# Kernel tuning notes

Hardware: AMD Instinct MI355X
Metric: run time of the kernel (lower is better)

Reference implementation:

```python
import jax, jax.numpy as jnp
import numpy as np

KG_E = 50000
KG_R = 500
E_DIM = 300
NE = 400000      # entity-entity adjacency nnz
NEER = 400000    # entity-entity-relation triples
ALPHA1 = 0.1
ALPHA2 = 0.3
LRELU_ALPHA = 0.2


def setup_inputs() -> dict:
    key = jax.random.key(0)
    ks = jax.random.split(key, 13)
    primal_e_0 = jax.random.normal(ks[0], (KG_E, E_DIM), jnp.float32)
    # sparse-ish relation->entity incidence matrices (dense storage as in torch code)
    r_head = (jax.random.uniform(ks[1], (KG_R, KG_E)) < 0.01).astype(jnp.float32)
    r_tail = (jax.random.uniform(ks[2], (KG_R, KG_E)) < 0.01).astype(jnp.float32)
    e_adj_index = jax.random.randint(ks[3], (2, NE), 0, KG_E)
    e_adj_data = jax.random.uniform(ks[4], (NE,), jnp.float32)
    eer_adj_index = jax.random.randint(ks[5], (2, NEER), 0, KG_E)
    eer_adj_data = jax.random.randint(ks[6], (NEER,), 0, KG_R)
    s = 0.05
    be_L = jax.random.normal(ks[7], (KG_E, 1), jnp.float32) * s
    be_R = jax.random.normal(ks[8], (KG_E, 1), jnp.float32) * s
    atten_r = jax.random.normal(ks[9], (2 * E_DIM, 1), jnp.float32) * s
    gcnW1 = jax.random.normal(ks[10], (E_DIM, E_DIM), jnp.float32) * s
    highwayWr = jax.random.normal(ks[11], (E_DIM, E_DIM), jnp.float32) * s
    highwaybr = jax.random.normal(ks[12], (E_DIM, 1), jnp.float32) * s
    return {"primal_e_0": primal_e_0, "r_head": r_head, "r_tail": r_tail,
            "e_adj_data": e_adj_data, "be_L": be_L, "be_R": be_R,
            "atten_r": atten_r, "gcnW1": gcnW1, "highwayWr": highwayWr,
            "highwaybr": highwaybr, "e_adj_index": e_adj_index,
            "eer_adj_index": eer_adj_index, "eer_adj_data": eer_adj_data}


def _spmm(idx, data, x):
    # sparse [KG_E, KG_E] (COO rows=idx[0], cols=idx[1], vals=data) @ dense x
    rows, cols = idx[0], idx[1]
    return jax.ops.segment_sum(data[:, None] * x[cols], rows, num_segments=KG_E)


def _inv_or_zero(x):
    return jnp.where(x == 0, 0.0, 1.0 / x)


def _add_r_layer(e, be_L, be_R, r_head, r_tail, rh_inv, rt_inv):
    L_r = (r_head @ (e * be_L)) * rh_inv   # [KG_R, E_DIM]
    R_r = (r_tail @ (e * be_R)) * rt_inv
    return jax.nn.relu(jnp.concatenate([L_r, R_r], axis=-1))  # [KG_R, 2*E_DIM]


def _add_e_att_layer(e, r_layer, eer_idx, eer_rel, atten_r):
    rows, cols = eer_idx[0], eer_idx[1]
    e_ij = jnp.concatenate([e[rows], e[cols]], axis=1)           # [NEER, 2*E_DIM]
    eer_embed = e_ij * r_layer[eer_rel]                           # [NEER, 2*E_DIM]
    score = (eer_embed @ atten_r)[:, 0]                           # [NEER]
    ee_atten = jnp.exp(-jax.nn.leaky_relu(score, LRELU_ALPHA))
    e_rowsum = jax.ops.segment_sum(ee_atten, rows, num_segments=KG_E)[:, None]
    e_rowsum = _inv_or_zero(e_rowsum)
    e_out = jax.ops.segment_sum(ee_atten[:, None] * e[cols], rows, num_segments=KG_E)
    return jax.nn.relu(e_out * e_rowsum)


def _add_diag_layer(e, gcnW1, e_adj_index, e_adj_data):
    # dropout p=0 (eval) -> identity
    return jax.nn.relu(_spmm(e_adj_index, e_adj_data, e @ gcnW1))


def _highway(e1, e2, Wr, br):
    gate = jax.nn.sigmoid(e1 @ Wr + br[:, 0])
    return gate * e2 + (1.0 - gate) * e1


def reference(primal_e_0, r_head, r_tail, e_adj_data, be_L, be_R, atten_r,
              gcnW1, highwayWr, highwaybr, e_adj_index, eer_adj_index,
              eer_adj_data):
    rh_inv = _inv_or_zero(jnp.sum(r_head, axis=-1, keepdims=True))
    rt_inv = _inv_or_zero(jnp.sum(r_tail, axis=-1, keepdims=True))
    name_embed = primal_e_0
    r1 = _add_r_layer(name_embed, be_L, be_R, r_head, r_tail, rh_inv, rt_inv)
    e1 = _add_e_att_layer(name_embed, r1, eer_adj_index, eer_adj_data, atten_r)
    e1 = name_embed + ALPHA1 * e1
    r2 = _add_r_layer(e1, be_L, be_R, r_head, r_tail, rh_inv, rt_inv)
    e2 = _add_e_att_layer(e1, r2, eer_adj_index, eer_adj_data, atten_r)
    e2 = name_embed + ALPHA2 * e2
    g1 = _add_diag_layer(e2, gcnW1, e_adj_index, e_adj_data)
    g2 = _highway(e2, g1, highwayWr, highwaybr)
    g3 = _add_diag_layer(g2, gcnW1, e_adj_index, e_adj_data)
    return _highway(g2, g3, highwayWr, highwaybr)
```

## Files before the change

kernel.cpp:

```cpp
#include <hip/hip_runtime.h>
#include <hip/hip_fp16.h>
#include <math.h>

#define KG_E  50000
#define KG_R  500
#define E_DIM 300
#define NPAIR 150
#define NP2   75
#define CAP   1024
#define LRELU 0.2f

#define NK    10
#define NT    40
#define XS_LD 328

#define NB_SCAN 49

typedef __attribute__((ext_vector_type(8))) _Float16 f16x8;
typedef __attribute__((ext_vector_type(4))) float f32x4;

__device__ __forceinline__ __half2 u2h2(unsigned u) {
  union { unsigned u; __half2 h; } v; v.u = u; return v.h;
}
__device__ __forceinline__ unsigned h22u(__half2 h) {
  union { unsigned u; __half2 h; } v; v.h = h; return v.u;
}
__device__ __forceinline__ float hlo(unsigned u) { return __low2float(u2h2(u)); }
__device__ __forceinline__ float hhi(unsigned u) { return __high2float(u2h2(u)); }
__device__ __forceinline__ unsigned packh(float lo, float hi) {
  return h22u(__floats2half2_rn(lo, hi));
}

__global__ __launch_bounds__(256) void k_toh(
    const float* __restrict__ src, __half* __restrict__ dst, int n4)
{
  int i = blockIdx.x * 256 + threadIdx.x;
  if (i >= n4) return;
  float4 f = ((const float4*)src)[i];
  uint2 o;
  o.x = packh(f.x, f.y);
  o.y = packh(f.z, f.w);
  ((uint2*)dst)[i] = o;
}

#define NCH 5
#define SCAP 1024
#define NF4 2500
__global__ __launch_bounds__(256) void k_compact2(
    const float* __restrict__ r_head, const float* __restrict__ r_tail,
    const float* __restrict__ be_L, const float* __restrict__ be_R,
    int* __restrict__ lidx, float* __restrict__ lsval,
    int* __restrict__ fill, float* __restrict__ rsum)
{
  __shared__ int   ls_e[SCAP];
  __shared__ float ls_v[SCAP];
  __shared__ int   ls_cnt;
  __shared__ float ls_sum;
  __shared__ int   ls_base;
  int m = blockIdx.z;
  int r = blockIdx.y;
  const float* rowp = (m ? r_tail : r_head) + (size_t)r * KG_E;
  const float* be   = m ? be_R : be_L;
  int slot = m * KG_R + r;
  int lane = threadIdx.x & 63;
  if (threadIdx.x == 0) { ls_cnt = 0; ls_sum = 0.f; }
  __syncthreads();

  const int CH = KG_E / NCH;
  int c0 = blockIdx.x * CH;
  const float4* rp4 = (const float4*)(rowp + c0);

  float vals[48];
  #pragma unroll
  for (int t = 0; t < 12; ++t) {
    int fi = t * 256 + threadIdx.x;
    float4 f = (fi < NF4) ? rp4[fi] : make_float4(0.f, 0.f, 0.f, 0.f);
    vals[t*4+0] = f.x; vals[t*4+1] = f.y; vals[t*4+2] = f.z; vals[t*4+3] = f.w;
  }
  float lsum = 0.f;
  int cnt = 0;
  #pragma unroll
  for (int q = 0; q < 48; ++q) {
    lsum += vals[q];
    cnt += (vals[q] != 0.f) ? 1 : 0;
  }
  int pre = cnt;
  #pragma unroll
  for (int off = 1; off < 64; off <<= 1) {
    int u = __shfl_up(pre, off, 64);
    if (lane >= off) pre += u;
  }
  int wave_base = 0;
  if (lane == 63 && pre > 0) wave_base = atomicAdd(&ls_cnt, pre);
  wave_base = __shfl(wave_base, 63, 64);
  if (cnt > 0) {
    int o = wave_base + pre - cnt;
    #pragma unroll
    for (int t = 0; t < 12; ++t) {
      int fi = t * 256 + threadIdx.x;
      #pragma unroll
      for (int q = 0; q < 4; ++q) {
        float v = vals[t*4+q];
        if (v != 0.f) {
          if (o < SCAP) {
            int e = c0 + fi * 4 + q;
            ls_e[o] = e;
            ls_v[o] = v * be[e];
          }
          ++o;
        }
      }
    }
  }
  #pragma unroll
  for (int off = 32; off > 0; off >>= 1) lsum += __shfl_xor(lsum, off, 64);
  if (lane == 0 && lsum != 0.f) atomicAdd(&ls_sum, lsum);
  __syncthreads();

  int total = ls_cnt < SCAP ? ls_cnt : SCAP;
  if (threadIdx.x == 0) {
    ls_base = atomicAdd(&fill[slot], total);
    if (ls_sum != 0.f) atomicAdd(&rsum[slot], ls_sum);
  }
  __syncthreads();
  int gbase = ls_base;
  int*   li = lidx  + (size_t)slot * CAP;
  float* lv = lsval + (size_t)slot * CAP;
  for (int i = threadIdx.x; i < total; i += 256) {
    int pos = gbase + i;
    if (pos < CAP) { li[pos] = ls_e[i]; lv[pos] = ls_v[i]; }
  }
}

__global__ __launch_bounds__(256) void k_rmeta(
    const int* __restrict__ fill, const float* __restrict__ rsum,
    int* __restrict__ cnt, float* __restrict__ inv)
{
  int i = blockIdx.x * 256 + threadIdx.x;
  if (i < 2 * KG_R) {
    int c = fill[i];
    cnt[i] = c > CAP ? CAP : c;
    float s = rsum[i];
    inv[i] = (s == 0.f) ? 0.f : 1.f / s;
  }
}

__global__ __launch_bounds__(192) void k_rlayer(
    const __half* __restrict__ Eb, const int* __restrict__ lidx,
    const float* __restrict__ lsval, const int* __restrict__ cnt,
    const float* __restrict__ inv, const float* __restrict__ atten,
    unsigned* __restrict__ wpk)
{
  int b = blockIdx.x;
  int m = b / KG_R, r = b % KG_R;
  int p = threadIdx.x;
  if (p >= NPAIR) return;
  int slot = m * KG_R + r;
  int n = cnt[slot];
  const int*   li = lidx  + (size_t)slot * CAP;
  const float* lv = lsval + (size_t)slot * CAP;
  float alo = 0.f, ahi = 0.f;
  #pragma unroll 4
  for (int i = 0; i < n; ++i) {
    int e = li[i];
    float s = lv[i];
    unsigned u = ((const unsigned*)(Eb + (size_t)e * E_DIM))[p];
    alo += s * hlo(u);
    ahi += s * hhi(u);
  }
  float iv = inv[slot];
  float vlo = alo * iv; vlo = vlo > 0.f ? vlo : 0.f;
  float vhi = ahi * iv; vhi = vhi > 0.f ? vhi : 0.f;
  vlo *= atten[m * E_DIM + 2 * p];
  vhi *= atten[m * E_DIM + 2 * p + 1];
  wpk[(size_t)slot * NPAIR + p] = packh(vlo, vhi);
}

__global__ __launch_bounds__(256) void k_hist(
    const int* __restrict__ rows, int* __restrict__ cnt, int n)
{
  int i = blockIdx.x * 256 + threadIdx.x;
  if (i < n) atomicAdd(&cnt[rows[i]], 1);
}

__global__ __launch_bounds__(256) void k_scan_a(
    const int* __restrict__ c0, const int* __restrict__ c1,
    int* __restrict__ bsum, int n)
{
  const int* c = blockIdx.y ? c1 : c0;
  int base = blockIdx.x * 1024;
  int s = 0;
  #pragma unroll
  for (int k = 0; k < 4; ++k) {
    int i = base + k * 256 + threadIdx.x;
    if (i < n) s += c[i];
  }
  #pragma unroll
  for (int off = 32; off > 0; off >>= 1) s += __shfl_xor(s, off, 64);
  __shared__ int ws[4];
  if ((threadIdx.x & 63) == 0) ws[threadIdx.x >> 6] = s;
  __syncthreads();
  if (threadIdx.x == 0)
    bsum[blockIdx.y * (NB_SCAN + 1) + blockIdx.x] = ws[0] + ws[1] + ws[2] + ws[3];
}

__global__ __launch_bounds__(64) void k_scan_b(int* __restrict__ bsum)
{
  if (threadIdx.x < 2) {
    int* b = bsum + threadIdx.x * (NB_SCAN + 1);
    int acc = 0;
    for (int i = 0; i < NB_SCAN; ++i) { int v = b[i]; b[i] = acc; acc += v; }
    b[NB_SCAN] = acc;
  }
}

__global__ __launch_bounds__(256) void k_scan_c(
    const int* __restrict__ c0, const int* __restrict__ c1,
    const int* __restrict__ bsum,
    int* __restrict__ s0, int* __restrict__ s1, int n)
{
  const int* c = blockIdx.y ? c1 : c0;
  int* sO = blockIdx.y ? s1 : s0;
  if (blockIdx.x == 0 && threadIdx.x == 0)
    sO[n] = bsum[blockIdx.y * (NB_SCAN + 1) + NB_SCAN];
  int boff = bsum[blockIdx.y * (NB_SCAN + 1) + blockIdx.x];
  int i0 = blockIdx.x * 1024 + threadIdx.x * 4;
  int4 v = {0, 0, 0, 0};
  if (i0 < n) v = ((const int4*)c)[i0 >> 2];
  int tsum = v.x + v.y + v.z + v.w;
  int lane = threadIdx.x & 63, wid = threadIdx.x >> 6;
  int inc = tsum;
  #pragma unroll
  for (int off = 1; off < 64; off <<= 1) {
    int u = __shfl_up(inc, off, 64);
    if (lane >= off) inc += u;
  }
  __shared__ int ws[4];
  if (lane == 63) ws[wid] = inc;
  __syncthreads();
  int woff = 0;
  if (wid > 0) woff += ws[0];
  if (wid > 1) woff += ws[1];
  if (wid > 2) woff += ws[2];
  int ex = boff + woff + inc - tsum;
  if (i0 < n) {
    int4 o;
    o.x = ex; o.y = ex + v.x; o.z = o.y + v.y; o.w = o.z + v.z;
    ((int4*)sO)[i0 >> 2] = o;
  }
}

__global__ __launch_bounds__(256) void k_scatter_eer(
    const int* __restrict__ eidx, const int* __restrict__ erel,
    const int* __restrict__ start, int* __restrict__ fill,
    int* __restrict__ scol, int* __restrict__ srel, int neer)
{
  int i = blockIdx.x * 256 + threadIdx.x;
  if (i >= neer) return;
  int row = eidx[i];
  int pos = start[row] + atomicAdd(&fill[row], 1);
  scol[pos] = eidx[neer + i];
  srel[pos] = erel[i];
}

__global__ __launch_bounds__(256) void k_scatter_adj(
    const int* __restrict__ aidx, const float* __restrict__ adata,
    const int* __restrict__ start, int* __restrict__ fill,
    int* __restrict__ scol, float* __restrict__ sval, int ne)
{
  int i = blockIdx.x * 256 + threadIdx.x;
  if (i >= ne) return;
  int row = aidx[i];
  int pos = start[row] + atomicAdd(&fill[row], 1);
  scol[pos] = aidx[ne + i];
  sval[pos] = adata[i];
}

__global__ __launch_bounds__(256) void k_att_csr(
    const __half* __restrict__ Eb, const unsigned* __restrict__ wpk,
    const int* __restrict__ start, const int* __restrict__ scol,
    const int* __restrict__ srel, const __half* __restrict__ baseb,
    float alpha, __half* __restrict__ outb)
{
  int wave = threadIdx.x >> 6, lane = threadIdx.x & 63;
  int half = lane >> 5, hl = lane & 31;
  int row = blockIdx.x * 4 + wave;
  if (row >= KG_E) return;
  int s = start[row], e = start[row + 1];
  const uint2* erp = (const uint2*)(Eb + (size_t)row * E_DIM);
  __half2 zero2 = __floats2half2_rn(0.f, 0.f);
  __half2 er[3][2], ac[3][2];
  #pragma unroll
  for (int c = 0; c < 3; ++c) {
    int m = c * 32 + hl;
    if (m < NP2) {
      uint2 u = erp[m];
      er[c][0] = u2h2(u.x); er[c][1] = u2h2(u.y);
    } else { er[c][0] = zero2; er[c][1] = zero2; }
    ac[c][0] = zero2; ac[c][1] = zero2;
  }
  float rs = 0.f;
  int nIter = (e - s + 1) >> 1;

  bool actA = false; int relA = 0;
  uint2 CA[3];
  #pragma unroll
  for (int c = 0; c < 3; ++c) CA[c] = make_uint2(0u, 0u);
  {
    int j0 = s + half;
    if (nIter > 0 && j0 < e) {
      actA = true;
      int col = scol[j0]; relA = srel[j0];
      const uint2* ecp = (const uint2*)(Eb + (size_t)col * E_DIM);
      #pragma unroll
      for (int c = 0; c < 3; ++c) {
        int m = c * 32 + hl;
        if (m < NP2) CA[c] = ecp[m];
      }
    }
  }

  for (int it = 0; it < nIter; ++it) {
    bool actB = false; int relB = 0;
    uint2 CB[3];
    #pragma unroll
    for (int c = 0; c < 3; ++c) CB[c] = make_uint2(0u, 0u);
    {
      int jn = s + 2 * (it + 1) + half;
      if (it + 1 < nIter && jn < e) {
        actB = true;
        int col = scol[jn]; relB = srel[jn];
        const uint2* ecp = (const uint2*)(Eb + (size_t)col * E_DIM);
        #pragma unroll
        for (int c = 0; c < 3; ++c) {
          int m = c * 32 + hl;
          if (m < NP2) CB[c] = ecp[m];
        }
      }
    }
    const uint2* whp = (const uint2*)(wpk + (size_t)relA * NPAIR);
    const uint2* wtp = (const uint2*)(wpk + (size_t)(KG_R + relA) * NPAIR);
    __half2 p2a = zero2, p2b = zero2;
    #pragma unroll
    for (int c = 0; c < 3; ++c) {
      int m = c * 32 + hl;
      if (m < NP2) {
        uint2 uh = whp[m], ut = wtp[m];
        p2a = __hfma2(er[c][0], u2h2(uh.x), p2a);
        p2b = __hfma2(er[c][1], u2h2(uh.y), p2b);
        p2a = __hfma2(u2h2(CA[c].x), u2h2(ut.x), p2a);
        p2b = __hfma2(u2h2(CA[c].y), u2h2(ut.y), p2b);
      }
    }
    __half2 p2 = __hadd2(p2a, p2b);
    float p4 = __low2float(p2) + __high2float(p2);
    #pragma unroll
    for (int off = 16; off > 0; off >>= 1) p4 += __shfl_xor(p4, off, 64);
    float la = p4 >= 0.f ? p4 : LRELU * p4;
    float at = actA ? __expf(-la) : 0.f;
    rs += at;
    __half2 at2 = __float2half2_rn(at);
    #pragma unroll
    for (int c = 0; c < 3; ++c) {
      ac[c][0] = __hfma2(at2, u2h2(CA[c].x), ac[c][0]);
      ac[c][1] = __hfma2(at2, u2h2(CA[c].y), ac[c][1]);
    }
    actA = actB; relA = relB;
    #pragma unroll
    for (int c = 0; c < 3; ++c) CA[c] = CB[c];
  }
  rs += __shfl_xor(rs, 32, 64);
  #pragma unroll
  for (int c = 0; c < 3; ++c) {
    #pragma unroll
    for (int k = 0; k < 2; ++k) {
      unsigned o = __shfl_xor(h22u(ac[c][k]), 32, 64);
      ac[c][k] = __hadd2(ac[c][k], u2h2(o));
    }
  }
  if (half == 0) {
    float iv = (rs == 0.f) ? 0.f : 1.f / rs;
    const uint2* bp = (const uint2*)(baseb + (size_t)row * E_DIM);
    uint2* op = (uint2*)(outb + (size_t)row * E_DIM);
    #pragma unroll
    for (int c = 0; c < 3; ++c) {
      int m = c * 32 + hl;
      if (m < NP2) {
        uint2 ub = bp[m];
        float v0 = __low2float(ac[c][0]) * iv;  v0 = v0 > 0.f ? v0 : 0.f;
        float v1 = __high2float(ac[c][0]) * iv; v1 = v1 > 0.f ? v1 : 0.f;
        float v2 = __low2float(ac[c][1]) * iv;  v2 = v2 > 0.f ? v2 : 0.f;
        float v3 = __high2float(ac[c][1]) * iv; v3 = v3 > 0.f ? v3 : 0.f;
        uint2 o2;
        o2.x = packh(hlo(ub.x) + alpha * v0, hhi(ub.x) + alpha * v1);
        o2.y = packh(hlo(ub.y) + alpha * v2, hhi(ub.y) + alpha * v3);
        op[m] = o2;
      }
    }
  }
}

__global__ __launch_bounds__(256) void k_spmm_hw(
    const __half* __restrict__ Xb, const int* __restrict__ start,
    const int* __restrict__ scol, const float* __restrict__ sval,
    const __half* __restrict__ Gb, const __half* __restrict__ baseb,
    const float* __restrict__ br,
    __half* __restrict__ outb, float* __restrict__ outf)
{
  int wave = threadIdx.x >> 6, lane = threadIdx.x & 63;
  int half = lane >> 5, hl = lane & 31;
  int row = blockIdx.x * 4 + wave;
  if (row >= KG_E) return;
  int s = start[row], e = start[row + 1];
  float ac0[3] = {0,0,0}, ac1[3] = {0,0,0}, ac2[3] = {0,0,0}, ac3[3] = {0,0,0};
  int nIter = (e - s + 1) >> 1;

  float vA = 0.f;
  uint2 XA[3];
  #pragma unroll
  for (int c = 0; c < 3; ++c) XA[c] = make_uint2(0u, 0u);
  {
    int j0 = s + half;
    if (nIter > 0 && j0 < e) {
      int col = scol[j0]; vA = sval[j0];
      const uint2* xp = (const uint2*)(Xb + (size_t)col * E_DIM);
      #pragma unroll
      for (int c = 0; c < 3; ++c) {
        int m = c * 32 + hl;
        if (m < NP2) XA[c] = xp[m];
      }
    }
  }
  for (int it = 0; it < nIter; ++it) {
    float vB = 0.f;
    uint2 XB[3];
    #pragma unroll
    for (int c = 0; c < 3; ++c) XB[c] = make_uint2(0u, 0u);
    {
      int jn = s + 2 * (it + 1) + half;
      if (it + 1 < nIter && jn < e) {
        int col = scol[jn]; vB = sval[jn];
        const uint2* xp = (const uint2*)(Xb + (size_t)col * E_DIM);
        #pragma unroll
        for (int c = 0; c < 3; ++c) {
          int m = c * 32 + hl;
          if (m < NP2) XB[c] = xp[m];
        }
      }
    }
    #pragma unroll
    for (int c = 0; c < 3; ++c) {
      ac0[c] += vA * hlo(XA[c].x); ac1[c] += vA * hhi(XA[c].x);
      ac2[c] += vA * hlo(XA[c].y); ac3[c] += vA * hhi(XA[c].y);
    }
    vA = vB;
    #pragma unroll
    for (int c = 0; c < 3; ++c) XA[c] = XB[c];
  }
  #pragma unroll
  for (int c = 0; c < 3; ++c) {
    ac0[c] += __shfl_xor(ac0[c], 32, 64);
    ac1[c] += __shfl_xor(ac1[c], 32, 64);
    ac2[c] += __shfl_xor(ac2[c], 32, 64);
    ac3[c] += __shfl_xor(ac3[c], 32, 64);
  }
  if (half == 0) {
    const uint2* gp = (const uint2*)(Gb + (size_t)row * E_DIM);
    const uint2* bp = (const uint2*)(baseb + (size_t)row * E_DIM);
    #pragma unroll
    for (int c = 0; c < 3; ++c) {
      int m = c * 32 + hl;
      if (m < NP2) {
        uint2 ug = gp[m], ub = bp[m];
        float4 b4 = ((const float4*)br)[m];
        float g0 = 1.f / (1.f + __expf(-(hlo(ug.x) + b4.x)));
        float g1 = 1.f / (1.f + __expf(-(hhi(ug.x) + b4.y)));
        float g2 = 1.f / (1.f + __expf(-(hlo(ug.y) + b4.z)));
        float g3 = 1.f / (1.f + __expf(-(hhi(ug.y) + b4.w)));
        float y0 = ac0[c] > 0.f ? ac0[c] : 0.f;
        float y1 = ac1[c] > 0.f ? ac1[c] : 0.f;
        float y2 = ac2[c] > 0.f ? ac2[c] : 0.f;
        float y3 = ac3[c] > 0.f ? ac3[c] : 0.f;
        float o0 = g0 * y0 + (1.f - g0) * hlo(ub.x);
        float o1 = g1 * y1 + (1.f - g1) * hhi(ub.x);
        float o2 = g2 * y2 + (1.f - g2) * hlo(ub.y);
        float o3 = g3 * y3 + (1.f - g3) * hhi(ub.y);
        if (outb) {
          uint2 ov;
          ov.x = packh(o0, o1); ov.y = packh(o2, o3);
          ((uint2*)(outb + (size_t)row * E_DIM))[m] = ov;
        } else {
          float4 of; of.x = o0; of.y = o1; of.z = o2; of.w = o3;
          ((float4*)(outf + (size_t)row * E_DIM))[m] = of;
        }
      }
    }
  }
}

__global__ __launch_bounds__(64) void k_packW(
    const float* __restrict__ W1, const float* __restrict__ W2,
    __half* __restrict__ Wp)
{
  int lane = threadIdx.x;
  int t = blockIdx.x, s = blockIdx.y;
  int c = t * 16 + (lane & 15);
  __half v[8];
  #pragma unroll
  for (int j = 0; j < 8; ++j) {
    int k = s * 32 + (lane >> 4) * 8 + j;
    float x = 0.f;
    if (k < E_DIM && c < 2 * E_DIM)
      x = (c < E_DIM) ? W1[(size_t)k * E_DIM + c]
                      : W2[(size_t)k * E_DIM + (c - E_DIM)];
    v[j] = __float2half_rn(x);
  }
  size_t base = ((size_t)(t * NK + s) * 64 + lane) * 8;
  #pragma unroll
  for (int j = 0; j < 8; ++j) Wp[base + j] = v[j];
}

__global__ __launch_bounds__(256) void k_gemm2_mfma(
    const __half* __restrict__ Xb, const __half* __restrict__ Wp,
    __half* __restrict__ Y1, __half* __restrict__ Y2, int M)
{
  __shared__ __half Xs[32][XS_LD];
  int tid = threadIdx.x;
  int r0 = blockIdx.x * 32;
  int nb = blockIdx.y;

  for (int t = tid; t < 32 * (XS_LD / 2); t += 256) {
    int r = t / (XS_LD / 2), u = t % (XS_LD / 2);
    unsigned v = 0;
    int rg = r0 + r;
    if (rg < M && u < E_DIM / 2) v = ((const unsigned*)Xb)[(size_t)rg * (E_DIM / 2) + u];
    ((unsigned*)&Xs[0][0])[r * (XS_LD / 2) + u] = v;
  }
  __syncthreads();

  int wid = tid >> 6, lane = tid & 63;
  int wave_m = wid >> 1, wave_n = wid & 1;
  int rowA = wave_m * 16 + (lane & 15);
  int kgrp = (lane >> 4) * 8;
  int tb0 = nb * 8 + wave_n * 4;

  const f16x8* wfrag = (const f16x8*)Wp + (size_t)tb0 * (NK * 64) + lane;

  f32x4 acc[4] = {{0,0,0,0},{0,0,0,0},{0,0,0,0},{0,0,0,0}};
  #pragma unroll 2
  for (int ks = 0; ks < NK; ++ks) {
    f16x8 a = *(const f16x8*)&Xs[rowA][ks * 32 + kgrp];
    #pragma unroll
    for (int nt = 0; nt < 4; ++nt) {
      f16x8 b = wfrag[(nt * NK + ks) * 64];
      acc[nt] = __builtin_amdgcn_mfma_f32_16x16x32_f16(a, b, acc[nt], 0, 0, 0);
    }
  }

  int rbase = r0 + wave_m * 16 + ((lane >> 4) << 2);
  #pragma unroll
  for (int nt = 0; nt < 4; ++nt) {
    int c = (tb0 + nt) * 16 + (lane & 15);
    #pragma unroll
    for (int j = 0; j < 4; ++j) {
      int row = rbase + j;
      if (row < M) {
        __half hv = __float2half_rn(acc[nt][j]);
        if (c < E_DIM)            Y1[(size_t)row * E_DIM + c] = hv;
        else if (c < 2 * E_DIM)   Y2[(size_t)row * E_DIM + (c - E_DIM)] = hv;
      }
    }
  }
}

extern "C" void kernel_launch(void* const* d_in, const int* in_sizes, int n_in,
                              void* d_out, int out_size, void* d_ws, size_t ws_size,
                              hipStream_t stream)
{
  const float* primal      = (const float*)d_in[0];
  const float* r_head      = (const float*)d_in[1];
  const float* r_tail      = (const float*)d_in[2];
  const float* e_adj_data  = (const float*)d_in[3];
  const float* be_L        = (const float*)d_in[4];
  const float* be_R        = (const float*)d_in[5];
  const float* atten_r     = (const float*)d_in[6];
  const float* gcnW1       = (const float*)d_in[7];
  const float* hwWr        = (const float*)d_in[8];
  const float* hwbr        = (const float*)d_in[9];
  const int*   e_adj_index = (const int*)d_in[10];
  const int*   eer_idx     = (const int*)d_in[11];
  const int*   eer_rel     = (const int*)d_in[12];
  int ne   = in_sizes[10] / 2;
  int neer = in_sizes[11] / 2;

  char* ws = (char*)d_ws;
  size_t off = 0;
  auto take = [&](size_t bytes) {
    void* p = ws + off;
    off = (off + bytes + 255) & ~(size_t)255;
    return p;
  };
  int*   cnt      = (int*)  take((size_t)2 * KG_R * sizeof(int));
  float* inv      = (float*)take((size_t)2 * KG_R * sizeof(float));
  size_t z0 = off;
  int*   hcntA    = (int*)  take((size_t)KG_E * sizeof(int));
  int*   hcntB    = (int*)  take((size_t)KG_E * sizeof(int));
  int*   hfillA   = (int*)  take((size_t)KG_E * sizeof(int));
  int*   hfillB   = (int*)  take((size_t)KG_E * sizeof(int));
  int*   rfill    = (int*)  take((size_t)2 * KG_R * sizeof(int));
  float* rsumb    = (float*)take((size_t)2 * KG_R * sizeof(float));
  size_t z1 = off;
  int*   lidx     = (int*)  take((size_t)2 * KG_R * CAP * sizeof(int));
  float* lsv      = (float*)take((size_t)2 * KG_R * CAP * sizeof(float));
  unsigned* wpk   = (unsigned*)take((size_t)2 * KG_R * NPAIR * sizeof(unsigned));
  int*   bsum     = (int*)  take((size_t)2 * (NB_SCAN + 1) * sizeof(int));
  int*   eer_start= (int*)  take((size_t)(KG_E + 4) * sizeof(int));
  int*   adj_start= (int*)  take((size_t)(KG_E + 4) * sizeof(int));
  int*   eer_scol = (int*)  take((size_t)neer * sizeof(int));
  int*   eer_srel = (int*)  take((size_t)neer * sizeof(int));
  int*   adj_scol = (int*)  take((size_t)ne * sizeof(int));
  float* adj_sval = (float*)take((size_t)ne * sizeof(float));
  __half* Wp = (__half*)take((size_t)NT * NK * 64 * 8 * sizeof(__half));
  __half* B0 = (__half*)take((size_t)KG_E * E_DIM * sizeof(__half));
  __half* B1 = (__half*)take((size_t)KG_E * E_DIM * sizeof(__half));
  __half* B2 = (__half*)take((size_t)KG_E * E_DIM * sizeof(__half));
  __half* Fb = (__half*)take((size_t)KG_E * E_DIM * sizeof(__half));
  __half* Gb = (__half*)take((size_t)KG_E * E_DIM * sizeof(__half));
  float* out      = (float*)d_out;
  (void)ws_size; (void)n_in; (void)out_size;

  int eg = (neer + 255) / 256;
  int ag = (ne + 255) / 256;

  hipMemsetAsync(ws + z0, 0, z1 - z0, stream);

  k_hist<<<eg, 256, 0, stream>>>(eer_idx, hcntA, neer);
  k_hist<<<ag, 256, 0, stream>>>(e_adj_index, hcntB, ne);
  k_scan_a<<<dim3(NB_SCAN, 2), 256, 0, stream>>>(hcntA, hcntB, bsum, KG_E);
  k_scan_b<<<1, 64, 0, stream>>>(bsum);
  k_scan_c<<<dim3(NB_SCAN, 2), 256, 0, stream>>>(hcntA, hcntB, bsum,
                                                 eer_start, adj_start, KG_E);
  k_scatter_eer<<<eg, 256, 0, stream>>>(eer_idx, eer_rel, eer_start, hfillA,
                                        eer_scol, eer_srel, neer);
  k_scatter_adj<<<ag, 256, 0, stream>>>(e_adj_index, e_adj_data, adj_start, hfillB,
                                        adj_scol, adj_sval, ne);

  k_compact2<<<dim3(NCH, KG_R, 2), 256, 0, stream>>>(r_head, r_tail, be_L, be_R,
                                                     lidx, lsv, rfill, rsumb);
  k_rmeta<<<(2 * KG_R + 255) / 256, 256, 0, stream>>>(rfill, rsumb, cnt, inv);
  k_packW<<<dim3(NT, NK), 64, 0, stream>>>(gcnW1, hwWr, Wp);
  int n4 = KG_E * E_DIM / 4;
  k_toh<<<(n4 + 255) / 256, 256, 0, stream>>>(primal, B0, n4);

  int rg = (KG_E + 3) / 4;

  k_rlayer<<<2 * KG_R, 192, 0, stream>>>(B0, lidx, lsv, cnt, inv, atten_r, wpk);
  k_att_csr<<<rg, 256, 0, stream>>>(B0, wpk, eer_start, eer_scol, eer_srel,
                                    B0, 0.1f, B1);
  k_rlayer<<<2 * KG_R, 192, 0, stream>>>(B1, lidx, lsv, cnt, inv, atten_r, wpk);
  k_att_csr<<<rg, 256, 0, stream>>>(B1, wpk, eer_start, eer_scol, eer_srel,
                                    B0, 0.3f, B2);

  dim3 gg((KG_E + 31) / 32, 5);
  k_gemm2_mfma<<<gg, 256, 0, stream>>>(B2, Wp, Fb, Gb, KG_E);
  k_spmm_hw<<<rg, 256, 0, stream>>>(Fb, adj_start, adj_scol, adj_sval,
                                    Gb, B2, hwbr, B1, (float*)nullptr);

  k_gemm2_mfma<<<gg, 256, 0, stream>>>(B1, Wp, Fb, Gb, KG_E);
  k_spmm_hw<<<rg, 256, 0, stream>>>(Fb, adj_start, adj_scol, adj_sval,
                                    Gb, B1, hwbr, (__half*)nullptr, out);
}
```

Baseline: 767.8 us.

## Split compaction rows into more chunks and retile GEMM waves to 2x2 MFMA blocks

The relation-row compaction kernel now splits each row into 10 chunks instead of 5, so each thread holds fewer values in registers and more blocks run in parallel. The GEMM kernel changes its wave tiling from 16 rows by 4 column tiles per wave to 32 rows by 2 column tiles per wave. Each loaded B fragment is now reused across two A fragments, which halves per-wave global weight-fragment loads in exchange for one extra LDS read per k-step. The added compaction blocks raise the count of shared atomic merges.

Measured after the change: 731.0 us (median of 2 runs). 4.8% less time.

```diff
diff --git a/kernel.cpp b/kernel.cpp
--- a/kernel.cpp
+++ b/kernel.cpp
@@ -43,9 +43,9 @@
   ((uint2*)dst)[i] = o;
 }
 
-#define NCH 5
+#define NCH 10
 #define SCAP 1024
-#define NF4 2500
+#define NF4 1250
 __global__ __launch_bounds__(256) void k_compact2(
     const float* __restrict__ r_head, const float* __restrict__ r_tail,
     const float* __restrict__ be_L, const float* __restrict__ be_R,
@@ -70,9 +70,9 @@
   int c0 = blockIdx.x * CH;
   const float4* rp4 = (const float4*)(rowp + c0);
 
-  float vals[48];
-  #pragma unroll
-  for (int t = 0; t < 12; ++t) {
+  float vals[20];
+  #pragma unroll
+  for (int t = 0; t < 5; ++t) {
     int fi = t * 256 + threadIdx.x;
     float4 f = (fi < NF4) ? rp4[fi] : make_float4(0.f, 0.f, 0.f, 0.f);
     vals[t*4+0] = f.x; vals[t*4+1] = f.y; vals[t*4+2] = f.z; vals[t*4+3] = f.w;
@@ -80,7 +80,7 @@
   float lsum = 0.f;
   int cnt = 0;
   #pragma unroll
-  for (int q = 0; q < 48; ++q) {
+  for (int q = 0; q < 20; ++q) {
     lsum += vals[q];
     cnt += (vals[q] != 0.f) ? 1 : 0;
   }
@@ -96,7 +96,7 @@
   if (cnt > 0) {
     int o = wave_base + pre - cnt;
     #pragma unroll
-    for (int t = 0; t < 12; ++t) {
+    for (int t = 0; t < 5; ++t) {
       int fi = t * 256 + threadIdx.x;
       #pragma unroll
       for (int q = 0; q < 4; ++q) {
@@ -539,35 +539,40 @@
   __syncthreads();
 
   int wid = tid >> 6, lane = tid & 63;
-  int wave_m = wid >> 1, wave_n = wid & 1;
-  int rowA = wave_m * 16 + (lane & 15);
+  int rowA = lane & 15;
   int kgrp = (lane >> 4) * 8;
-  int tb0 = nb * 8 + wave_n * 4;
-
-  const f16x8* wfrag = (const f16x8*)Wp + (size_t)tb0 * (NK * 64) + lane;
-
-  f32x4 acc[4] = {{0,0,0,0},{0,0,0,0},{0,0,0,0},{0,0,0,0}};
+  int tbase = nb * 8 + wid * 2;
+
+  const f16x8* wf0 = (const f16x8*)Wp + (size_t)tbase * (NK * 64) + lane;
+  const f16x8* wf1 = (const f16x8*)Wp + (size_t)(tbase + 1) * (NK * 64) + lane;
+
+  f32x4 acc[2][2] = {{{0,0,0,0},{0,0,0,0}},{{0,0,0,0},{0,0,0,0}}};
   #pragma unroll 2
   for (int ks = 0; ks < NK; ++ks) {
-    f16x8 a = *(const f16x8*)&Xs[rowA][ks * 32 + kgrp];
-    #pragma unroll
-    for (int nt = 0; nt < 4; ++nt) {
-      f16x8 b = wfrag[(nt * NK + ks) * 64];
-      acc[nt] = __builtin_amdgcn_mfma_f32_16x16x32_f16(a, b, acc[nt], 0, 0, 0);
-    }
-  }
-
-  int rbase = r0 + wave_m * 16 + ((lane >> 4) << 2);
-  #pragma unroll
-  for (int nt = 0; nt < 4; ++nt) {
-    int c = (tb0 + nt) * 16 + (lane & 15);
-    #pragma unroll
-    for (int j = 0; j < 4; ++j) {
-      int row = rbase + j;
-      if (row < M) {
-        __half hv = __float2half_rn(acc[nt][j]);
-        if (c < E_DIM)            Y1[(size_t)row * E_DIM + c] = hv;
-        else if (c < 2 * E_DIM)   Y2[(size_t)row * E_DIM + (c - E_DIM)] = hv;
+    f16x8 a0 = *(const f16x8*)&Xs[rowA][ks * 32 + kgrp];
+    f16x8 a1 = *(const f16x8*)&Xs[16 + rowA][ks * 32 + kgrp];
+    f16x8 b0 = wf0[ks * 64];
+    f16x8 b1 = wf1[ks * 64];
+    acc[0][0] = __builtin_amdgcn_mfma_f32_16x16x32_f16(a0, b0, acc[0][0], 0, 0, 0);
+    acc[0][1] = __builtin_amdgcn_mfma_f32_16x16x32_f16(a0, b1, acc[0][1], 0, 0, 0);
+    acc[1][0] = __builtin_amdgcn_mfma_f32_16x16x32_f16(a1, b0, acc[1][0], 0, 0, 0);
+    acc[1][1] = __builtin_amdgcn_mfma_f32_16x16x32_f16(a1, b1, acc[1][1], 0, 0, 0);
+  }
+
+  int rquad = (lane >> 4) << 2;
+  #pragma unroll
+  for (int mg = 0; mg < 2; ++mg) {
+    #pragma unroll
+    for (int nt = 0; nt < 2; ++nt) {
+      int c = (tbase + nt) * 16 + (lane & 15);
+      #pragma unroll
+      for (int j = 0; j < 4; ++j) {
+        int row = r0 + mg * 16 + rquad + j;
+        if (row < M) {
+          __half hv = __float2half_rn(acc[mg][nt][j]);
+          if (c < E_DIM)            Y1[(size_t)row * E_DIM + c] = hv;
+          else if (c < 2 * E_DIM)   Y2[(size_t)row * E_DIM + (c - E_DIM)] = hv;
+        }
       }
     }
   }
```
